# Kernel tuning notes

Measured on AMD Instinct MI355X. Metric: run time of the kernel, lower is better.

## Reference

```python
import jax, jax.numpy as jnp
import numpy as np

WAVELET_LEN = 64
N_SCALES = 8
MIN_SCALE, MAX_SCALE = 1.0, 32.0
SPARSITY_THRESHOLD = 1e-4


def _morlet_bank():
    # matches AdaptiveWaveletTransform._initialize_mother_wavelets
    t = jnp.linspace(-4.0, 4.0, WAVELET_LEN)
    i = jnp.arange(N_SCALES, dtype=jnp.float32)
    omega = 2.0 + i * 0.5           # [n_scales]
    sigma = 1.0 + i * 0.1
    w = jnp.exp(-t[None, :] ** 2 / (2.0 * sigma[:, None] ** 2)) * jnp.cos(omega[:, None] * t[None, :])
    return w / jnp.linalg.norm(w, axis=1, keepdims=True)  # [n_scales, 64]


def setup_inputs() -> dict:
    key = jax.random.key(0)
    signal = jax.random.normal(key, (16, 4096, 64), dtype=jnp.float32)
    mother_wavelets = _morlet_bank().astype(jnp.float32)   # learned param
    scale_weights = jnp.ones((N_SCALES,), dtype=jnp.float32)  # learned param
    return {"signal": signal, "mother_wavelets": mother_wavelets, "scale_weights": scale_weights}


def reference(signal, mother_wavelets, scale_weights):
    # scales are static (registered buffer) -> compute in numpy
    scales = np.logspace(np.log10(MIN_SCALE), np.log10(MAX_SCALE), N_SCALES)
    B, S, F = signal.shape
    per_scale = []
    grid = jnp.arange(WAVELET_LEN, dtype=jnp.float32)
    for idx in range(N_SCALES):
        scale = float(scales[idx])
        L = int(WAVELET_LEN * scale)  # dilated kernel length (static)
        # F.interpolate(mode='linear', align_corners=True): sample at linspace(0, 63, L)
        xq = jnp.linspace(0.0, WAVELET_LEN - 1.0, L)
        kern = jnp.interp(xq, grid, mother_wavelets[idx]) / np.sqrt(scale)  # [L]
        n = S + L - 1                      # full conv length
        n_fft = 1 << int(np.ceil(np.log2(n)))  # next pow2 (static)
        # vectorized FFT conv over batch and features simultaneously
        sig_f = jnp.fft.rfft(signal, n=n_fft, axis=1)      # [B, n_fft//2+1, F]
        k_f = jnp.fft.rfft(kern, n=n_fft)                   # [n_fft//2+1]
        conv = jnp.fft.irfft(sig_f * k_f[None, :, None], n=n_fft, axis=1)
        per_scale.append(conv[:, :S, :])   # L>=64 so n>=S always
    coeffs = jnp.stack(per_scale, axis=1)  # [B, n_scales, S, F]
    coeffs = coeffs * scale_weights[None, :, None, None]
    # use_sparse + eval-mode thresholding
    mask = (jnp.abs(coeffs) > SPARSITY_THRESHOLD).astype(coeffs.dtype)
    return coeffs * mask
```

## Files before the change

kernel.cpp:

```cpp
#include <hip/hip_runtime.h>
#include <hip/hip_bf16.h>
#include <math.h>

#define S_LEN 4096
#define N_FEAT 64
#define N_BATCH 16
#define N_SCALES 8
#define THRESH 1e-4f
#define PADL 2048
#define NCHUNK ((PADL + S_LEN) / 16)
#define BCHUNK_ELEMS 1024

typedef unsigned short ushort_t;
typedef __attribute__((ext_vector_type(8))) short bf16x8;
typedef __attribute__((ext_vector_type(16))) float f32x16;

struct ScaleParams {
    int L[N_SCALES], Mc[N_SCALES], Niter[N_SCALES], Aoff[N_SCALES];
    float inv_sqrt_scale[N_SCALES], step[N_SCALES];
};

__global__ void prep_A(const float* __restrict__ mother, ushort_t* __restrict__ Atab,
                       ScaleParams p, int totalA) {
    int i = blockIdx.x * blockDim.x + threadIdx.x;
    if (i >= totalA) return;
    int idx = 0;
#pragma unroll
    for (int s = 1; s < N_SCALES; ++s)
        if (i >= p.Aoff[s]) idx = s;
    int rel = i - p.Aoff[idx];
    int ci = rel >> 9;
    int r = rel & 511;
    int lane = r >> 3, e = r & 7;
    int ti = lane & 31, sj = 8 * (lane >> 5) + e;
    int kidx = 16 * (ci - 2) - 16 + ti - sj;
    float v = 0.f;
    if (kidx >= 0 && kidx < p.L[idx]) {
        float xq = fminf(kidx * p.step[idx], 63.0f);
        int i0 = (int)xq; if (i0 > 62) i0 = 62;
        float frac = xq - (float)i0;
        float a = mother[idx * 64 + i0];
        float b = mother[idx * 64 + i0 + 1];
        v = (a + (b - a) * frac) * p.inv_sqrt_scale[idx];
    }
    __hip_bfloat16 hh = __float2bfloat16(v);
    Atab[i] = *reinterpret_cast<ushort_t*>(&hh);
}

__global__ __launch_bounds__(256) void transpose_sig(const float* __restrict__ sig,
                                                     ushort_t* __restrict__ XTc) {
    const int b = blockIdx.y;
    const int G = blockIdx.x * 4 + (threadIdx.x >> 6);
    const int l = threadIdx.x & 63;
    unsigned int u[4];
    if (G < PADL / 8) {
        u[0] = u[1] = u[2] = u[3] = 0u;
    } else {
        const float* sp = sig + ((size_t)b * S_LEN + ((size_t)G * 8 - PADL)) * N_FEAT + l;
#pragma unroll
        for (int j = 0; j < 4; ++j) {
            float v0 = sp[(size_t)(2 * j) * N_FEAT];
            float v1 = sp[(size_t)(2 * j + 1) * N_FEAT];
            __hip_bfloat16 h0 = __float2bfloat16(v0);
            __hip_bfloat16 h1 = __float2bfloat16(v1);
            u[j] = (unsigned int)*reinterpret_cast<ushort_t*>(&h0) |
                   ((unsigned int)*reinterpret_cast<ushort_t*>(&h1) << 16);
        }
    }
    uint4 vv = {u[0], u[1], u[2], u[3]};
    *reinterpret_cast<uint4*>(XTc + (size_t)b * (NCHUNK * BCHUNK_ELEMS)
                              + (size_t)G * 512 + l * 8) = vv;
}

#define MFMA(A, X, C) C = __builtin_amdgcn_mfma_f32_32x32x16_bf16(A, X, C, 0, 0, 0)

__global__ __launch_bounds__(256, 4) void wavelet_mfma(
    const ushort_t* __restrict__ XTc, const ushort_t* __restrict__ Atab,
    const float* __restrict__ sw, float* __restrict__ out, ScaleParams p) {
    const int n = blockIdx.x;
    const int xcd = n & 7;
    const int r = n >> 3;
    const int b = 2 * xcd + (r & 1);
    const int q = r >> 1;
    const int xblk = q & 15;
    const int idx = 7 - (q >> 4);

    const int wave = threadIdx.x >> 6, lane = threadIdx.x & 63;
    const int tw0 = xblk * 256 + wave * 64;
    const int h = lane >> 5, fc = lane & 31;
    const int niter = p.Niter[idx];
    const int c0 = (PADL + tw0) / 16 + 1;

    const ushort_t* Ab = Atab + p.Aoff[idx] + lane * 8;
    const ushort_t* Bb = XTc + (size_t)b * (NCHUNK * BCHUNK_ELEMS)
                       + h * 512 + fc * 8;

    f32x16 c00, c01, c10, c11;
#pragma unroll
    for (int i = 0; i < 16; ++i) { c00[i] = 0.f; c01[i] = 0.f; c10[i] = 0.f; c11[i] = 0.f; }

    bf16x8 Ar[4];
#pragma unroll
    for (int i = 0; i < 4; ++i)
        Ar[i] = *reinterpret_cast<const bf16x8*>(Ab + i * 512);
    bf16x8 Xe0 = *reinterpret_cast<const bf16x8*>(Bb + (size_t)(c0 + 2) * 1024);
    bf16x8 Xe1 = *reinterpret_cast<const bf16x8*>(Bb + (size_t)(c0 + 2) * 1024 + 256);
    bf16x8 Xo0 = *reinterpret_cast<const bf16x8*>(Bb + (size_t)(c0 + 1) * 1024);
    bf16x8 Xo1 = *reinterpret_cast<const bf16x8*>(Bb + (size_t)(c0 + 1) * 1024 + 256);

    const ushort_t* Apf = Ab + 4 * 512;
    const ushort_t* Bpf = Bb + (size_t)c0 * 1024;

    for (int it = 0; it < niter; it += 8) {
#pragma unroll
        for (int ph = 0; ph < 8; ++ph) {
            bf16x8 a0 = Ar[ph & 3];
            bf16x8 a1 = Ar[(ph + 2) & 3];
            bf16x8 x0 = (ph & 1) ? Xo0 : Xe0;
            bf16x8 x1 = (ph & 1) ? Xo1 : Xe1;
            Ar[ph & 3] = *reinterpret_cast<const bf16x8*>(Apf);
            Apf += 512;
            if (ph & 1) {
                Xo0 = *reinterpret_cast<const bf16x8*>(Bpf);
                Xo1 = *reinterpret_cast<const bf16x8*>(Bpf + 256);
            } else {
                Xe0 = *reinterpret_cast<const bf16x8*>(Bpf);
                Xe1 = *reinterpret_cast<const bf16x8*>(Bpf + 256);
            }
            Bpf -= 1024;
            MFMA(a0, x0, c00); MFMA(a0, x1, c01);
            MFMA(a1, x0, c10); MFMA(a1, x1, c11);
        }
    }

    const float w = sw[idx];
    float* ob = out + ((size_t)(b * N_SCALES + idx) * S_LEN + tw0) * N_FEAT + fc;
#define STORE_TILE(CLO, CHI, JT)                                               \
    {                                                                          \
        _Pragma("unroll") for (int i = 0; i < 16; ++i) {                       \
            const int row = (JT) * 32 + (i & 3) + 8 * (i >> 2) + 4 * h;        \
            float v;                                                           \
            v = CLO[i] * w;                                                    \
            ob[(size_t)row * N_FEAT]      = (fabsf(v) > THRESH) ? v : 0.f;     \
            v = CHI[i] * w;                                                    \
            ob[(size_t)row * N_FEAT + 32] = (fabsf(v) > THRESH) ? v : 0.f;     \
        }                                                                      \
    }
    STORE_TILE(c00, c01, 0)
    STORE_TILE(c10, c11, 1)
#undef STORE_TILE
}

extern "C" void kernel_launch(void* const* d_in, const int* in_sizes, int n_in,
                              void* d_out, int out_size, void* d_ws, size_t ws_size,
                              hipStream_t stream) {
    const float* sig    = (const float*)d_in[0];
    const float* mother = (const float*)d_in[1];
    const float* sw     = (const float*)d_in[2];
    float* out = (float*)d_out;

    ushort_t* Atab = (ushort_t*)((char*)d_ws + 32768);
    ushort_t* XTc  = (ushort_t*)((char*)d_ws + 524288);

    ScaleParams p;
    int aoff = 0;
    for (int i = 0; i < N_SCALES; ++i) {
        double scale = pow(10.0, (double)i * log10(32.0) / 7.0);
        double v = 64.0 * scale;
        double r = floor(v + 0.5);
        int L = (fabs(v - r) < 1e-6) ? (int)r : (int)v;
        p.L[i] = L;
        p.Mc[i] = (L + 46) >> 4;
        p.Niter[i] = (p.Mc[i] + 9) & ~7;
        p.Aoff[i] = aoff;
        aoff += (p.Niter[i] + 8) * 512;
        p.inv_sqrt_scale[i] = (float)(1.0 / sqrt(scale));
        p.step[i] = (float)(63.0 / (double)(L - 1));
    }
    const int totalA = aoff;

    prep_A<<<dim3((totalA + 255) / 256), dim3(256), 0, stream>>>(
        mother, Atab, p, totalA);
    transpose_sig<<<dim3((PADL + S_LEN) / 32, N_BATCH), dim3(256), 0, stream>>>(
        sig, XTc);

    wavelet_mfma<<<dim3(S_LEN / 256 * N_BATCH * N_SCALES), dim3(256), 0, stream>>>(
        XTc, Atab, sw, out, p);
}
```

Measured before the change: 74.84 us.

## Split long-kernel scales across waves with split-K and LDS reduction for load balance

Blocks for the large scales (6,7) now split the reduction over kernel taps across 4 waves and scales 4,5 across 2 waves, with partial accumulators summed in shared memory before the thresholded store. The grid grows from 2048 to 4096 blocks. The goal is to even out the per-block work, since the longest scales previously dominated the tail. The cost is extra LDS traffic, two barriers per block and more blocks overall.

Result: slower. 78.86 us (+5.4%).

```diff
diff --git a/kernel.cpp b/kernel.cpp
--- a/kernel.cpp
+++ b/kernel.cpp
@@ -82,13 +82,23 @@
     const int r = n >> 3;
     const int b = 2 * xcd + (r & 1);
     const int q = r >> 1;
-    const int xblk = q & 15;
-    const int idx = 7 - (q >> 4);
+    int idx, ks, tu0;
+    if (q < 128)      { idx = 7 - (q >> 6);         ks = 4; tu0 = q & 63; }
+    else if (q < 192) { idx = 5 - ((q - 128) >> 5); ks = 2; tu0 = ((q - 128) & 31) * 2; }
+    else              { idx = 3 - ((q - 192) >> 4); ks = 1; tu0 = ((q - 192) & 15) * 4; }
 
     const int wave = threadIdx.x >> 6, lane = threadIdx.x & 63;
-    const int tw0 = xblk * 256 + wave * 64;
+    int tunit, seg;
+    if (ks == 4)      { tunit = tu0;               seg = wave; }
+    else if (ks == 2) { tunit = tu0 + (wave >> 1); seg = wave & 1; }
+    else              { tunit = tu0 + wave;        seg = 0; }
+
+    const int tw0 = tunit * 64;
     const int h = lane >> 5, fc = lane & 31;
     const int niter = p.Niter[idx];
+    const int G = niter >> 3;
+    const int ms = ((seg * G) / ks) * 8;
+    const int me = (((seg + 1) * G) / ks) * 8;
     const int c0 = (PADL + tw0) / 16 + 1;
 
     const ushort_t* Ab = Atab + p.Aoff[idx] + lane * 8;
@@ -102,16 +112,16 @@
     bf16x8 Ar[4];
 #pragma unroll
     for (int i = 0; i < 4; ++i)
-        Ar[i] = *reinterpret_cast<const bf16x8*>(Ab + i * 512);
-    bf16x8 Xe0 = *reinterpret_cast<const bf16x8*>(Bb + (size_t)(c0 + 2) * 1024);
-    bf16x8 Xe1 = *reinterpret_cast<const bf16x8*>(Bb + (size_t)(c0 + 2) * 1024 + 256);
-    bf16x8 Xo0 = *reinterpret_cast<const bf16x8*>(Bb + (size_t)(c0 + 1) * 1024);
-    bf16x8 Xo1 = *reinterpret_cast<const bf16x8*>(Bb + (size_t)(c0 + 1) * 1024 + 256);
-
-    const ushort_t* Apf = Ab + 4 * 512;
-    const ushort_t* Bpf = Bb + (size_t)c0 * 1024;
-
-    for (int it = 0; it < niter; it += 8) {
+        Ar[i] = *reinterpret_cast<const bf16x8*>(Ab + (size_t)(ms + i) * 512);
+    bf16x8 Xe0 = *reinterpret_cast<const bf16x8*>(Bb + (size_t)(c0 + 2 - ms) * 1024);
+    bf16x8 Xe1 = *reinterpret_cast<const bf16x8*>(Bb + (size_t)(c0 + 2 - ms) * 1024 + 256);
+    bf16x8 Xo0 = *reinterpret_cast<const bf16x8*>(Bb + (size_t)(c0 + 1 - ms) * 1024);
+    bf16x8 Xo1 = *reinterpret_cast<const bf16x8*>(Bb + (size_t)(c0 + 1 - ms) * 1024 + 256);
+
+    const ushort_t* Apf = Ab + (size_t)(ms + 4) * 512;
+    const ushort_t* Bpf = Bb + (size_t)(c0 - ms) * 1024;
+
+    for (int it = ms; it < me; it += 8) {
 #pragma unroll
         for (int ph = 0; ph < 8; ++ph) {
             bf16x8 a0 = Ar[ph & 3];
@@ -134,21 +144,59 @@
     }
 
     const float w = sw[idx];
-    float* ob = out + ((size_t)(b * N_SCALES + idx) * S_LEN + tw0) * N_FEAT + fc;
+    __shared__ float buf[2][64][65];
+
+    if (ks == 1) {
+        float* ob = out + ((size_t)(b * N_SCALES + idx) * S_LEN + tw0) * N_FEAT + fc;
 #define STORE_TILE(CLO, CHI, JT)                                               \
-    {                                                                          \
-        _Pragma("unroll") for (int i = 0; i < 16; ++i) {                       \
-            const int row = (JT) * 32 + (i & 3) + 8 * (i >> 2) + 4 * h;        \
-            float v;                                                           \
-            v = CLO[i] * w;                                                    \
-            ob[(size_t)row * N_FEAT]      = (fabsf(v) > THRESH) ? v : 0.f;     \
-            v = CHI[i] * w;                                                    \
-            ob[(size_t)row * N_FEAT + 32] = (fabsf(v) > THRESH) ? v : 0.f;     \
-        }                                                                      \
-    }
-    STORE_TILE(c00, c01, 0)
-    STORE_TILE(c10, c11, 1)
+        {                                                                      \
+            _Pragma("unroll") for (int i = 0; i < 16; ++i) {                   \
+                const int row = (JT) * 32 + (i & 3) + 8 * (i >> 2) + 4 * h;    \
+                float v;                                                       \
+                v = CLO[i] * w;                                                \
+                ob[(size_t)row * N_FEAT]      = (fabsf(v) > THRESH) ? v : 0.f; \
+                v = CHI[i] * w;                                                \
+                ob[(size_t)row * N_FEAT + 32] = (fabsf(v) > THRESH) ? v : 0.f; \
+            }                                                                  \
+        }
+        STORE_TILE(c00, c01, 0)
+        STORE_TILE(c10, c11, 1)
 #undef STORE_TILE
+    } else {
+        const int ub = wave >> 1;
+#define PUT(ACC, J, F, OP)                                                     \
+        {                                                                      \
+            _Pragma("unroll") for (int i = 0; i < 16; ++i) {                   \
+                const int row = (J) * 32 + (i & 3) + 8 * (i >> 2) + 4 * h;     \
+                buf[ub][row][(F) * 32 + fc] OP ACC[i];                         \
+            }                                                                  \
+        }
+        if (!(wave & 1)) {
+            PUT(c00, 0, 0, =) PUT(c01, 0, 1, =) PUT(c10, 1, 0, =) PUT(c11, 1, 1, =)
+        }
+        __syncthreads();
+        if (wave & 1) {
+            PUT(c00, 0, 0, +=) PUT(c01, 0, 1, +=) PUT(c10, 1, 0, +=) PUT(c11, 1, 1, +=)
+        }
+        __syncthreads();
+#undef PUT
+        float* ob = out + ((size_t)(b * N_SCALES + idx) * S_LEN + tw0) * N_FEAT;
+        if (ks == 4) {
+#pragma unroll
+            for (int rr = 0; rr < 16; ++rr) {
+                const int row = wave * 16 + rr;
+                float v = (buf[0][row][lane] + buf[1][row][lane]) * w;
+                ob[(size_t)row * N_FEAT + lane] = (fabsf(v) > THRESH) ? v : 0.f;
+            }
+        } else {
+#pragma unroll
+            for (int rr = 0; rr < 32; ++rr) {
+                const int row = (wave & 1) * 32 + rr;
+                float v = buf[ub][row][lane] * w;
+                ob[(size_t)row * N_FEAT + lane] = (fabsf(v) > THRESH) ? v : 0.f;
+            }
+        }
+    }
 }
 
 extern "C" void kernel_launch(void* const* d_in, const int* in_sizes, int n_in,
@@ -184,6 +232,5 @@
     transpose_sig<<<dim3((PADL + S_LEN) / 32, N_BATCH), dim3(256), 0, stream>>>(
         sig, XTc);
 
-    wavelet_mfma<<<dim3(S_LEN / 256 * N_BATCH * N_SCALES), dim3(256), 0, stream>>>(
-        XTc, Atab, sw, out, p);
-}
+    wavelet_mfma<<<dim3(4096), dim3(256), 0, stream>>>(XTc, Atab, sw, out, p);
+}
```
